# Kernel tuning notes

Measured on AMD Instinct MI355X. Metric: run time of the kernel, lower is better.

## Reference

```python
import jax, jax.numpy as jnp
import numpy as np

SKIP_THRESHOLD = 0.3
NUM_HEADS = 16
TOP_K = 2


def _layernorm(x, g, b, eps=1e-6):
    m = jnp.mean(x, axis=-1, keepdims=True)
    v = jnp.var(x, axis=-1, keepdims=True)
    return (x - m) * jax.lax.rsqrt(v + eps) * g + b


def _silu(x):
    return x * jax.nn.sigmoid(x)


def _causal_dwconv(x, w):
    # x: [B,S,C], w: [k,C] depthwise causal conv
    k, S = w.shape[0], x.shape[1]
    xp = jnp.pad(x, ((0, 0), (k - 1, 0), (0, 0)))
    return sum(xp[:, i:i + S, :] * w[i] for i in range(k))


def _same_dwconv(x, w):
    k, S = w.shape[0], x.shape[1]
    pl = k // 2
    xp = jnp.pad(x, ((0, 0), (pl, k - 1 - pl), (0, 0)))
    return sum(xp[:, i:i + S, :] * w[i] for i in range(k))


def _mamba_block(x, w_in, conv_w, a_log, w_bc, w_dt, dt_bias, d_skip, w_out):
    # Selective-scan SSM (Mamba-style), O(L)
    B, S, D = x.shape
    d_inner = conv_w.shape[1]
    n = w_bc.shape[1] // 2
    xz = x @ w_in                                   # [B,S,2*d_inner]
    xc, z = xz[..., :d_inner], xz[..., d_inner:]
    xc = _silu(_causal_dwconv(xc, conv_w))
    bc = xc @ w_bc                                  # [B,S,2n]
    Bt, Ct = bc[..., :n], bc[..., n:]
    dt = jax.nn.softplus(xc * w_dt + dt_bias)       # [B,S,d_inner]
    A = -jnp.exp(a_log)                             # [d_inner]

    def step(h, inp):
        xc_t, dt_t, B_t, C_t = inp                  # [B,d_inner],[B,d_inner],[B,n],[B,n]
        decay = jnp.exp(dt_t * A)[..., None]        # [B,d_inner,1]
        h = decay * h + (dt_t * xc_t)[..., None] * B_t[:, None, :]
        y_t = jnp.einsum('bcn,bn->bc', h, C_t)
        return h, y_t

    h0 = jnp.zeros((B, d_inner, n), x.dtype)
    xs = (xc.transpose(1, 0, 2), dt.transpose(1, 0, 2),
          Bt.transpose(1, 0, 2), Ct.transpose(1, 0, 2))
    _, ys = jax.lax.scan(step, h0, xs)
    y = ys.transpose(1, 0, 2) + d_skip * xc
    return (y * _silu(z)) @ w_out


def _timecrystal_block(x, theta, w, b):
    # Energy-conserving rotation-style mixing
    return jnp.cos(theta) * x + jnp.sin(theta) * jnp.tanh(x @ w + b)


def _wlam_block(x, wq, wk, wv, wo, conv_w, nh):
    # Haar wavelet decomposition -> attention on approx coeffs -> reconstruct
    B, S, D = x.shape
    hd = D // nh
    inv = 0.7071067811865476
    xe, xo = x[:, 0::2], x[:, 1::2]
    a = (xe + xo) * inv                             # approx [B,S/2,D]
    det = (xe - xo) * inv                           # detail
    L = a.shape[1]
    q = (a @ wq).reshape(B, L, nh, hd)
    k = (a @ wk).reshape(B, L, nh, hd)
    v = (a @ wv).reshape(B, L, nh, hd)
    att = jnp.einsum('bqhd,bkhd->bhqk', q, k) * (1.0 / np.sqrt(hd))
    att = jax.nn.softmax(att, axis=-1)
    o = jnp.einsum('bhqk,bkhd->bqhd', att, v).reshape(B, L, D) @ wo
    xe2 = (o + det) * inv
    xo2 = (o - det) * inv
    y = jnp.stack([xe2, xo2], axis=2).reshape(B, S, D)
    return _same_dwconv(y, conv_w)


def _moe_block(x, wg, w1, b1, w2, b2, top_k):
    # Top-k sparse MoE; dense per-expert compute weighted by top-k gates
    B, S, D = x.shape
    E = wg.shape[1]
    xt = x.reshape(-1, D)
    logits = xt @ wg
    topv, topi = jax.lax.top_k(logits, top_k)
    w = jax.nn.softmax(topv, axis=-1)
    gates = (jax.nn.one_hot(topi, E, dtype=x.dtype) * w[..., None]).sum(axis=1)  # [T,E]
    y = jnp.zeros_like(xt)
    for e in range(E):
        h = jax.nn.gelu(xt @ w1[e] + b1[e])
        y = y + gates[:, e:e + 1] * (h @ w2[e] + b2[e])
    return y.reshape(B, S, D)


def setup_inputs() -> dict:
    key = jax.random.key(0)
    ks = jax.random.split(key, 20)
    B, S, D = 2, 2048, 1024
    DI, N, CK = 2 * D, 64, 4
    E, FF = 8, 4096
    NB = 4

    def rn(k, shape, scale=0.02):
        return jax.random.normal(k, shape, dtype=jnp.float32) * scale

    return {
        'hidden_states': jax.random.normal(ks[0], (B, S, D), jnp.float32),
        'router_w': rn(ks[1], (D, NB)),
        'router_b': jnp.zeros((NB,), jnp.float32),
        'ln_g': jnp.ones((NB, D), jnp.float32),
        'ln_b': jnp.zeros((NB, D), jnp.float32),
        'm_win': rn(ks[2], (D, 2 * DI)),
        'm_conv': rn(ks[3], (CK, DI), 0.1),
        'm_alog': jnp.zeros((DI,), jnp.float32),
        'm_wbc': rn(ks[4], (DI, 2 * N)),
        'm_wdt': rn(ks[5], (DI,)),
        'm_dtb': jnp.full((DI,), -1.0, jnp.float32),
        'm_dskip': jnp.ones((DI,), jnp.float32),
        'm_wout': rn(ks[6], (DI, D)),
        'tc_theta': jnp.array(0.5, jnp.float32),
        'tc_w': rn(ks[7], (D, D)),
        'tc_b': jnp.zeros((D,), jnp.float32),
        'w_q': rn(ks[8], (D, D)),
        'w_k': rn(ks[9], (D, D)),
        'w_v': rn(ks[10], (D, D)),
        'w_o': rn(ks[11], (D, D)),
        'wlam_conv': rn(ks[12], (4, D), 0.25),
        'moe_wg': rn(ks[13], (D, E)),
        'moe_w1': rn(ks[14], (E, D, FF)),
        'moe_b1': jnp.zeros((E, FF), jnp.float32),
        'moe_w2': rn(ks[15], (E, FF, D)),
        'moe_b2': jnp.zeros((E, D), jnp.float32),
    }


def reference(hidden_states, router_w, router_b, ln_g, ln_b,
              m_win, m_conv, m_alog, m_wbc, m_wdt, m_dtb, m_dskip, m_wout,
              tc_theta, tc_w, tc_b,
              w_q, w_k, w_v, w_o, wlam_conv,
              moe_wg, moe_w1, moe_b1, moe_w2, moe_b2):
    h = hidden_states
    # Adaptive block router: mean pool -> sigmoid scores -> hard skip mask (inference)
    pooled = jnp.mean(h, axis=1)                     # [B,D]
    scores = jax.nn.sigmoid(pooled @ router_w + router_b)  # [B,4]
    masks = (scores > SKIP_THRESHOLD).astype(h.dtype)

    h = h + masks[:, 0, None, None] * _mamba_block(
        _layernorm(h, ln_g[0], ln_b[0]), m_win, m_conv, m_alog, m_wbc,
        m_wdt, m_dtb, m_dskip, m_wout)
    h = h + masks[:, 1, None, None] * _timecrystal_block(
        _layernorm(h, ln_g[1], ln_b[1]), tc_theta, tc_w, tc_b)
    h = h + masks[:, 2, None, None] * _wlam_block(
        _layernorm(h, ln_g[2], ln_b[2]), w_q, w_k, w_v, w_o, wlam_conv, NUM_HEADS)
    h = h + masks[:, 3, None, None] * _moe_block(
        _layernorm(h, ln_g[3], ln_b[3]), moe_wg, moe_w1, moe_b1, moe_w2, moe_b2, TOP_K)
    return h
```

## Files before the change

### kernel.cpp

```cpp
#include <hip/hip_runtime.h>
#include <math.h>

#define S_LEN   2048
#define B_SZ    2
#define DM      1024
#define DI      2048
#define NST     64
#define LH      1024
#define NH      16
#define HD      64
#define TT      4096
#define NEXP    8
#define FF      4096
#define CHK     1024
#define MAXTILE 72
#define INVR2   0.7071067811865476f
#define CHUNK   128
#define NCH     16

#define OFF_POOLED 0
#define OFF_COUNTS 2048
#define OFF_CURSOR 2056
#define OFF_MASKS  2064
#define OFF_NTILE  2072
// ... 254 lines not shown
                                                 int ldi, int ldo) {
    __shared__ float t[64][65];
    const int tid = threadIdx.x;
    const int k0 = blockIdx.x << 6, n0 = blockIdx.y << 6;
    const int rr = tid >> 4, cc = (tid & 15) << 2;
#pragma unroll
    for (int i = 0; i < 4; ++i) {
        float4 v = *(const float4*)(in + (size_t)(k0 + rr + i * 16) * ldi + n0 + cc);
        *(float4*)&t[rr + i * 16][cc] = v;
    }
    __syncthreads();
#pragma unroll
    for (int i = 0; i < 4; ++i) {
        int n = rr + i * 16;
        ushort4 h4, m4, l4;
        split3v(t[cc + 0][n], h4.x, m4.x, l4.x);
        split3v(t[cc + 1][n], h4.y, m4.y, l4.y);
        split3v(t[cc + 2][n], h4.z, m4.z, l4.z);
        split3v(t[cc + 3][n], h4.w, m4.w, l4.w);
        size_t of = (size_t)(n0 + n) * ldo + k0 + cc;
        *(ushort4*)(oh + of) = h4;
        *(ushort4*)(om + of) = m4;
        *(ushort4*)(ol + of) = l4;
    }
}

__global__ __launch_bounds__(256) void transb_k(const float* __restrict__ in,
                                                unsigned short* __restrict__ out,
                                                int ldi, int ldo,
                                                long inStride, long outStride) {
    __shared__ float t[64][65];
    const int tid = threadIdx.x;
    in  += (size_t)blockIdx.z * inStride;
    out += (size_t)blockIdx.z * outStride;
    const int k0 = blockIdx.x << 6, n0 = blockIdx.y << 6;
    const int rr = tid >> 4, cc = (tid & 15) << 2;
#pragma unroll
    for (int i = 0; i < 4; ++i) {
        float4 v = *(const float4*)(in + (size_t)(k0 + rr + i * 16) * ldi + n0 + cc);
        *(float4*)&t[rr + i * 16][cc] = v;
    }
    __syncthreads();
#pragma unroll
    for (int i = 0; i < 4; ++i) {
        int n = rr + i * 16;
        ushort4 o;
        o.x = f2b(t[cc + 0][n]); o.y = f2b(t[cc + 1][n]);
        o.z = f2b(t[cc + 2][n]); o.w = f2b(t[cc + 3][n]);
        *(ushort4*)(out + (size_t)(n0 + n) * ldo + k0 + cc) = o;
    }
}

__global__ __launch_bounds__(256) void mmx3_k(const unsigned short* __restrict__ Ah,
                                              const unsigned short* __restrict__ Am,
                                              const unsigned short* __restrict__ Al,
                                              const unsigned short* __restrict__ Bh,
                                              const unsigned short* __restrict__ Bm,
                                              const unsigned short* __restrict__ Bl,
                                              float* __restrict__ C,
                                              int lda, int ldb, int ldc, int K) {
    __shared__ unsigned short S[6][4096];
    const int tid = threadIdx.x;
    const int m0 = (int)blockIdx.x << 7, n0 = (int)blockIdx.y << 7;
    size_t aoff[2], boff[2];
    int dst[2];
#pragma unroll
    for (int c = 0; c < 2; ++c) {
        int idx = tid + (c << 8);
        int r = idx >> 2, sd = idx & 3;
        int ks = (sd ^ (r & 3)) << 3;
        aoff[c] = (size_t)(m0 + r) * lda + ks;
        boff[c] = (size_t)(n0 + r) * ldb + ks;
        dst[c] = idx << 3;
    }
    const int lane = tid & 63;
    const int w = tid >> 6, wr = w >> 1, wc = w & 1;
    const int lrow = lane & 15, lgrp = lane >> 4;
    f4_t acc[4][4];
#pragma unroll
    for (int i = 0; i < 4; ++i)
#pragma unroll
        for (int j = 0; j < 4; ++j) acc[i][j] = (f4_t){0.f, 0.f, 0.f, 0.f};
    int ard[4], brd[4];
#pragma unroll
    for (int t4 = 0; t4 < 4; ++t4) {
        int ra = wr * 64 + t4 * 16 + lrow;
        ard[t4] = ra * 32 + ((lgrp ^ (ra & 3)) << 3);
        int rb = wc * 64 + t4 * 16 + lrow;
        brd[t4] = rb * 32 + ((lgrp ^ (rb & 3)) << 3);
    }
    for (int k0 = 0; k0 < K; k0 += 32) {
        __syncthreads();
#pragma unroll
        for (int c = 0; c < 2; ++c) {
            gld16(Ah + aoff[c] + k0, &S[0][dst[c]]);
            gld16(Am + aoff[c] + k0, &S[1][dst[c]]);
            gld16(Al + aoff[c] + k0, &S[2][dst[c]]);
            gld16(Bh + boff[c] + k0, &S[3][dst[c]]);
            gld16(Bm + boff[c] + k0, &S[4][dst[c]]);
            gld16(Bl + boff[c] + k0, &S[5][dst[c]]);
        }
        __syncthreads();
        bf8_t ah4[4], am4[4], al4[4];
#pragma unroll
        for (int t4 = 0; t4 < 4; ++t4) {
            ah4[t4] = *(const bf8_t*)&S[0][ard[t4]];
            am4[t4] = *(const bf8_t*)&S[1][ard[t4]];
            al4[t4] = *(const bf8_t*)&S[2][ard[t4]];
        }
#pragma unroll
        for (int ni = 0; ni < 4; ++ni) {
            bf8_t bh = *(const bf8_t*)&S[3][brd[ni]];
            bf8_t bm = *(const bf8_t*)&S[4][brd[ni]];
            bf8_t bl = *(const bf8_t*)&S[5][brd[ni]];
#pragma unroll
            for (int mi = 0; mi < 4; ++mi) {
                acc[mi][ni] = __builtin_amdgcn_mfma_f32_16x16x32_bf16(ah4[mi], bh, acc[mi][ni], 0, 0, 0);
                acc[mi][ni] = __builtin_amdgcn_mfma_f32_16x16x32_bf16(am4[mi], bh, acc[mi][ni], 0, 0, 0);
                acc[mi][ni] = __builtin_amdgcn_mfma_f32_16x16x32_bf16(al4[mi], bh, acc[mi][ni], 0, 0, 0);
                acc[mi][ni] = __builtin_amdgcn_mfma_f32_16x16x32_bf16(ah4[mi], bm, acc[mi][ni], 0, 0, 0);
                acc[mi][ni] = __builtin_amdgcn_mfma_f32_16x16x32_bf16(am4[mi], bm, acc[mi][ni], 0, 0, 0);
                acc[mi][ni] = __builtin_amdgcn_mfma_f32_16x16x32_bf16(ah4[mi], bl, acc[mi][ni], 0, 0, 0);
            }
        }
    }
#pragma unroll
    for (int mi = 0; mi < 4; ++mi) {
#pragma unroll
        for (int j = 0; j < 4; ++j) {
            int rr = wr * 64 + mi * 16 + lgrp * 4 + j;
#pragma unroll
            for (int ni = 0; ni < 4; ++ni) {
                int col = n0 + wc * 64 + ni * 16 + lrow;
                C[(size_t)(m0 + rr) * ldc + col] = acc[mi][ni][j];
            }
        }
    }
}

template<int MODE>
__global__ __launch_bounds__(256) void mm_k(const unsigned short* __restrict__ A,
                                            const unsigned short* __restrict__ Bt,
                                            void* __restrict__ Cv,
                                            int lda, int ldb, int ldc, int K,
                                            const float* __restrict__ bias, int fofs,
                                            const int* __restrict__ ntile,
                                            const int* __restrict__ tileE,
                                            const int* __restrict__ tileR,
                                            const int* __restrict__ tileC,
                                            const int* __restrict__ rtok) {
    __shared__ unsigned short As[8192];
    __shared__ unsigned short Bs[8192];
    const int tid = threadIdx.x;
    int m0 = 0;
    const int n0 = (int)blockIdx.y << 7;
    int cnt = 128, e = 0, row0 = 0;
    if constexpr (MODE >= 2) {
        if ((int)blockIdx.x >= ntile[0]) return;
        e = tileE[blockIdx.x]; row0 = tileR[blockIdx.x]; cnt = tileC[blockIdx.x];
    } else {
        m0 = (int)blockIdx.x << 7;
    }
    const unsigned short* Bp = Bt;
    if constexpr (MODE >= 2) Bp += (size_t)e << 20;
    size_t aoff[4], boff[4];
#pragma unroll
    for (int c = 0; c < 4; ++c) {
        int r = (tid >> 3) + 32 * c;
        int ks = ((tid & 7) ^ (r & 7)) << 3;
        int gr;
        if constexpr (MODE == 2)      gr = rtok[row0 + (r < cnt ? r : cnt - 1)];
        else if constexpr (MODE >= 3) gr = row0 + (r < cnt ? r : cnt - 1);
        else                          gr = m0 + r;
        aoff[c] = (size_t)gr * lda + ks;
        boff[c] = (size_t)(n0 + r) * ldb + ks;
    }
    const int lane = tid & 63;
    const int w = tid >> 6, wr = w >> 1, wc = w & 1;
    const int lrow = lane & 15, lgrp = lane >> 4;
    f4_t acc[4][4];
#pragma unroll
    for (int i = 0; i < 4; ++i)
#pragma unroll
        for (int j = 0; j < 4; ++j) acc[i][j] = (f4_t){0.f, 0.f, 0.f, 0.f};
    int ard[4][2], brd[4][2];
#pragma unroll
    for (int t4 = 0; t4 < 4; ++t4)
#pragma unroll
        for (int kk = 0; kk < 2; ++kk) {
            int ra = wr * 64 + t4 * 16 + lrow;
            ard[t4][kk] = ra * 64 + (((lgrp + (kk << 2)) ^ (ra & 7)) << 3);
            int rb = wc * 64 + t4 * 16 + lrow;
            brd[t4][kk] = rb * 64 + (((lgrp + (kk << 2)) ^ (rb & 7)) << 3);
        }
    for (int k0 = 0; k0 < K; k0 += 64) {
        __syncthreads();
#pragma unroll
        for (int c = 0; c < 4; ++c)
            gld16(A + aoff[c] + k0, As + c * 2048 + tid * 8);
#pragma unroll
        for (int c = 0; c < 4; ++c)
            gld16(Bp + boff[c] + k0, Bs + c * 2048 + tid * 8);
        __syncthreads();
        bf8_t af[4][2], bfv[4][2];
#pragma unroll
        for (int t4 = 0; t4 < 4; ++t4) {
            af[t4][0]  = *(const bf8_t*)&As[ard[t4][0]];
            af[t4][1]  = *(const bf8_t*)&As[ard[t4][1]];
            bfv[t4][0] = *(const bf8_t*)&Bs[brd[t4][0]];
            bfv[t4][1] = *(const bf8_t*)&Bs[brd[t4][1]];
        }
#pragma unroll
        for (int mi = 0; mi < 4; ++mi)
#pragma unroll
            for (int ni = 0; ni < 4; ++ni) {
                acc[mi][ni] = __builtin_amdgcn_mfma_f32_16x16x32_bf16(af[mi][0], bfv[ni][0], acc[mi][ni], 0, 0, 0);
                acc[mi][ni] = __builtin_amdgcn_mfma_f32_16x16x32_bf16(af[mi][1], bfv[ni][1], acc[mi][ni], 0, 0, 0);
            }
    }
#pragma unroll
    for (int mi = 0; mi < 4; ++mi) {
#pragma unroll
        for (int j = 0; j < 4; ++j) {
            int lr = wr * 64 + mi * 16 + lgrp * 4 + j;
            if constexpr (MODE >= 2) { if (lr >= cnt) continue; }
#pragma unroll
            for (int ni = 0; ni < 4; ++ni) {
                int col = n0 + wc * 64 + ni * 16 + lrow;
                float vv = acc[mi][ni][j];
                if constexpr (MODE == 0) {
                    ((float*)Cv)[(size_t)(m0 + lr) * ldc + col] = vv;
                } else if constexpr (MODE == 1) {
                    ((unsigned short*)Cv)[(size_t)(m0 + lr) * ldc + col] = f2b(vv);
                } else if constexpr (MODE == 2) {
                    float bz = bias[(size_t)e * FF + fofs + col];
                    ((unsigned short*)Cv)[(size_t)(row0 + lr) * ldc + col] = f2b(gelu_tanh(vv + bz));
                } else if constexpr (MODE == 3) {
                    ((float*)Cv)[(size_t)(row0 + lr) * ldc + col] += vv;
                } else {
                    ((float*)Cv)[(size_t)(row0 + lr) * ldc + col] = vv + bias[(size_t)e * DM + col];
                }
            }
        }
    }
}

__global__ __launch_bounds__(256) void gemmsk_f32(const float* __restrict__ A, int lda,
                                                  const float* __restrict__ B, int ldb,
                                                  float* __restrict__ P, int ldc, int Kslab) {
    __shared__ float As[16][68];
    __shared__ float Bs[16][68];
    const int tid = threadIdx.x;
    const int tx = tid & 15, ty = tid >> 4;
    const int m0 = blockIdx.x * 64, n0 = blockIdx.y * 64;
    const int kbeg = blockIdx.z * Kslab, kend = kbeg + Kslab;
    P += (size_t)blockIdx.z * 4096 * 128;
    const int la_r = tid >> 2, la_k = (tid & 3) << 2;
    const int lb_r = tid >> 4, lb_n = (tid & 15) << 2;
    float acc[4][4] = {};
    for (int k0 = kbeg; k0 < kend; k0 += 16) {
        float4 av = *(const float4*)(A + (size_t)(m0 + la_r) * lda + k0 + la_k);
        float4 bv = *(const float4*)(B + (size_t)(k0 + lb_r) * ldb + n0 + lb_n);
        __syncthreads();
        As[la_k + 0][la_r] = av.x; As[la_k + 1][la_r] = av.y;
        As[la_k + 2][la_r] = av.z; As[la_k + 3][la_r] = av.w;
        *(float4*)&Bs[lb_r][lb_n] = bv;
        __syncthreads();
#pragma unroll
        for (int kk = 0; kk < 16; ++kk) {
            float4 a4 = *(const float4*)&As[kk][ty << 2];
            float4 b4 = *(const float4*)&Bs[kk][tx << 2];
            float aa[4] = {a4.x, a4.y, a4.z, a4.w};
            float bb[4] = {b4.x, b4.y, b4.z, b4.w};
#pragma unroll
            for (int i = 0; i < 4; ++i)
#pragma unroll
                for (int j = 0; j < 4; ++j)
                    acc[i][j] = fmaf(aa[i], bb[j], acc[i][j]);
        }
    }
#pragma unroll
    for (int i = 0; i < 4; ++i) {
        int m = m0 + (ty << 2) + i;
        float4 o;
        o.x = acc[i][0]; o.y = acc[i][1]; o.z = acc[i][2]; o.w = acc[i][3];
        *(float4*)(P + (size_t)m * ldc + n0 + (tx << 2)) = o;
    }
}

__global__ __launch_bounds__(256) void wbc_red_k(const float* __restrict__ part,
                                                 float* __restrict__ bc) {
    size_t i = (size_t)blockIdx.x * 256 + threadIdx.x;
    float s = 0.f;
#pragma unroll
    for (int z = 0; z < 8; ++z) s += part[(size_t)z * 524288 + i];
    bc[i] = s;
}

__global__ __launch_bounds__(256) void mamba_conv_k(const float* __restrict__ xz,
                                                    const float* __restrict__ cw,
                                                    float* __restrict__ xc) {
    size_t i = (size_t)blockIdx.x * 256 + threadIdx.x;
    int c = (int)(i & (DI - 1));
    size_t row = i >> 11;
    int s = (int)(row & (S_LEN - 1));
    float acc = 0.f;
#pragma unroll
    for (int t = 0; t < 4; ++t) {
        int ss = s - 3 + t;
        if (ss >= 0) acc = fmaf(cw[t * DI + c], xz[(row - 3 + t) * 4096 + c], acc);
    }
    float sg = 1.f / (1.f + expf(-acc));
    xc[i] = acc * sg;
}

__global__ __launch_bounds__(256) void scan1_k(const float* __restrict__ xc,
                                               const float* __restrict__ bc,
                                               const float* __restrict__ alog,
                                               const float* __restrict__ wdt,
                                               const float* __restrict__ dtb,
                                               float* __restrict__ hend,
                                               float* __restrict__ pprod) {
    const int b = blockIdx.z, k = blockIdx.y;
    const int c = blockIdx.x * 256 + threadIdx.x;
    __shared__ float Bs[CHUNK][64];
    const int s0 = k * CHUNK;
    const float4* bc4 = (const float4*)(bc + ((size_t)(b * S_LEN + s0)) * 128);
    for (int idx = threadIdx.x; idx < CHUNK * 16; idx += 256) {
        int r = idx >> 4, q = idx & 15;
        *(float4*)&Bs[r][q << 2] = bc4[r * 32 + q];
    }
    __syncthreads();
    const float A = -expf(alog[c]);
    const float wdtc = wdt[c], dtbc = dtb[c];
    float hs[NST];
#pragma unroll
    for (int n = 0; n < NST; ++n) hs[n] = 0.f;
    float dtsum = 0.f;
    const float* xcp = xc + ((size_t)(b * S_LEN + s0)) * DI + c;
    for (int s = 0; s < CHUNK; ++s) {
        float xcv = xcp[(size_t)s * DI];
        float t = fmaf(xcv, wdtc, dtbc);
        float dtv = (t > 20.f) ? t : log1pf(expf(t));
        float decay = expf(dtv * A);
        float coef = dtv * xcv;
        dtsum += dtv;
#pragma unroll
        for (int n4 = 0; n4 < 16; ++n4) {
            float4 bv = *(const float4*)&Bs[s][n4 << 2];
            hs[n4 * 4 + 0] = fmaf(decay, hs[n4 * 4 + 0], coef * bv.x);
            hs[n4 * 4 + 1] = fmaf(decay, hs[n4 * 4 + 1], coef * bv.y);
            hs[n4 * 4 + 2] = fmaf(decay, hs[n4 * 4 + 2], coef * bv.z);
            hs[n4 * 4 + 3] = fmaf(decay, hs[n4 * 4 + 3], coef * bv.w);
        }
    }
    float* hp = hend + (((size_t)(b * NCH + k)) * DI + c) * NST;
#pragma unroll
    for (int n = 0; n < NST; n += 4) {
        float4 v; v.x = hs[n]; v.y = hs[n + 1]; v.z = hs[n + 2]; v.w = hs[n + 3];
        *(float4*)(hp + n) = v;
    }
    pprod[((size_t)(b * NCH + k)) * DI + c] = expf(dtsum * A);
}

__global__ __launch_bounds__(256) void scan2_k(const float* __restrict__ hend,
                                               const float* __restrict__ pprod,
                                               float* __restrict__ hin) {
    size_t g = (size_t)blockIdx.x * 256 + threadIdx.x;
    int n = (int)(g & 63);
    int c = (int)((g >> 6) & (DI - 1));
    int b = (int)(g >> 17);
    float h = 0.f;
    for (int k = 0; k < NCH; ++k) {
        size_t base = (size_t)(b * NCH + k) * DI + c;
        hin[base * NST + n] = h;
        h = fmaf(pprod[base], h, hend[base * NST + n]);
    }
}

__global__ __launch_bounds__(256) void scan3_k(float* __restrict__ xcio,
                                               const float* __restrict__ bc,
                                               const float* __restrict__ xz,
                                               const float* __restrict__ alog,
                                               const float* __restrict__ wdt,
                                               const float* __restrict__ dtb,
                                               const float* __restrict__ dskip,
                                               const float* __restrict__ hin) {
    const int b = blockIdx.z, k = blockIdx.y;
    const int c = blockIdx.x * 256 + threadIdx.x;
    __shared__ float Bs[CHUNK][64];
    __shared__ float Cs[CHUNK][64];
    const int s0 = k * CHUNK;
    const float4* bc4 = (const float4*)(bc + ((size_t)(b * S_LEN + s0)) * 128);
    for (int idx = threadIdx.x; idx < CHUNK * 32; idx += 256) {
        int r = idx >> 5, q = idx & 31;
        float4 v = bc4[r * 32 + q];
        if (q < 16) *(float4*)&Bs[r][q << 2] = v;
        else        *(float4*)&Cs[r][(q - 16) << 2] = v;
    }
    __syncthreads();
    const float A = -expf(alog[c]);
    const float wdtc = wdt[c], dtbc = dtb[c], skipc = dskip[c];
    float hs[NST];
    const float* hp = hin + (((size_t)(b * NCH + k)) * DI + c) * NST;
#pragma unroll
    for (int n = 0; n < NST; n += 4) {
        float4 v = *(const float4*)(hp + n);
        hs[n] = v.x; hs[n + 1] = v.y; hs[n + 2] = v.z; hs[n + 3] = v.w;
    }
    float* xcp = xcio + ((size_t)(b * S_LEN + s0)) * DI + c;
    const float* zp = xz + ((size_t)(b * S_LEN + s0)) * 4096 + DI + c;
    for (int s = 0; s < CHUNK; ++s) {
        float xcv = xcp[(size_t)s * DI];
        float t = fmaf(xcv, wdtc, dtbc);
        float dtv = (t > 20.f) ? t : log1pf(expf(t));
        float decay = expf(dtv * A);
        float coef = dtv * xcv;
        float y = 0.f;
#pragma unroll
        for (int n4 = 0; n4 < 16; ++n4) {
            float4 bv = *(const float4*)&Bs[s][n4 << 2];
            float4 cv = *(const float4*)&Cs[s][n4 << 2];
            float h0 = fmaf(decay, hs[n4 * 4 + 0], coef * bv.x);
            float h1 = fmaf(decay, hs[n4 * 4 + 1], coef * bv.y);
            float h2 = fmaf(decay, hs[n4 * 4 + 2], coef * bv.z);
            float h3 = fmaf(decay, hs[n4 * 4 + 3], coef * bv.w);
            hs[n4 * 4 + 0] = h0; hs[n4 * 4 + 1] = h1;
            hs[n4 * 4 + 2] = h2; hs[n4 * 4 + 3] = h3;
            y = fmaf(h0, cv.x, y); y = fmaf(h1, cv.y, y);
            y = fmaf(h2, cv.z, y); y = fmaf(h3, cv.w, y);
        }
        y = fmaf(skipc, xcv, y);
        float z = zp[(size_t)s * 4096];
        float sz = z / (1.f + expf(-z));
        xcp[(size_t)s * DI] = y * sz;
    }
}

__global__ __launch_bounds__(256) void wsplit_k(const float* __restrict__ ln,
                                                unsigned short* __restrict__ ah,
                                                unsigned short* __restrict__ am,
                                                unsigned short* __restrict__ al,
                                                float* __restrict__ det) {
    size_t f = (size_t)blockIdx.x * 256 + threadIdx.x;
    int d4 = (int)(f & 255);
    size_t l = f >> 8;
    size_t b = l >> 10;
    size_t li = l & 1023;
    const float4* ln4 = (const float4*)ln;
    float4 xe = ln4[(b * S_LEN + 2 * li) * 256 + d4];
    float4 xo = ln4[(b * S_LEN + 2 * li + 1) * 256 + d4];
    float4 av, dv;
    av.x = (xe.x + xo.x) * INVR2; dv.x = (xe.x - xo.x) * INVR2;
    av.y = (xe.y + xo.y) * INVR2; dv.y = (xe.y - xo.y) * INVR2;
    av.z = (xe.z + xo.z) * INVR2; dv.z = (xe.z - xo.z) * INVR2;
    av.w = (xe.w + xo.w) * INVR2; dv.w = (xe.w - xo.w) * INVR2;
    ushort4 h4, m4, l4;
    split3q(av, h4, m4, l4);
    ((ushort4*)ah)[f] = h4;
    ((ushort4*)am)[f] = m4;
    ((ushort4*)al)[f] = l4;
    ((float4*)det)[f] = dv;
}

__global__ __launch_bounds__(256) void wlam_attn_k(const float* __restrict__ q,
                                                   const float* __restrict__ k,
                                                   const float* __restrict__ v,
                                                   float* __restrict__ o0,
                                                   float* __restrict__ o1,
                                                   float* __restrict__ ml) {
    __shared__ float Qt[64][68];
    __shared__ float KPt[64][68];
    __shared__ float Vs[64][68];
    const int tid = threadIdx.x;
    const int b = blockIdx.z >> 1, half = blockIdx.z & 1;
    const int hh = blockIdx.y;
    const int q0 = blockIdx.x << 6;
    const int tx = tid & 15, ty = tid >> 4;
    const int sr = tid & 63, sc4 = (tid >> 6) << 4;
    {
        const float* qp = q + ((size_t)(b * LH + q0 + sr)) * DM + hh * HD + sc4;
        float4 v0 = *(const float4*)qp;
        float4 v1 = *(const float4*)(qp + 4);
        float4 v2 = *(const float4*)(qp + 8);
        float4 v3 = *(const float4*)(qp + 12);
        Qt[sc4 + 0][sr] = v0.x;  Qt[sc4 + 1][sr] = v0.y;  Qt[sc4 + 2][sr] = v0.z;  Qt[sc4 + 3][sr] = v0.w;
        Qt[sc4 + 4][sr] = v1.x;  Qt[sc4 + 5][sr] = v1.y;  Qt[sc4 + 6][sr] = v1.z;  Qt[sc4 + 7][sr] = v1.w;
        Qt[sc4 + 8][sr] = v2.x;  Qt[sc4 + 9][sr] = v2.y;  Qt[sc4 + 10][sr] = v2.z; Qt[sc4 + 11][sr] = v2.w;
        Qt[sc4 + 12][sr] = v3.x; Qt[sc4 + 13][sr] = v3.y; Qt[sc4 + 14][sr] = v3.z; Qt[sc4 + 15][sr] = v3.w;
    }
    float mrow[4] = {-INFINITY, -INFINITY, -INFINITY, -INFINITY};
    float lrow[4] = {0.f, 0.f, 0.f, 0.f};
    float oacc[4][4] = {};
    const int c0beg = half << 9;
    for (int c0 = c0beg; c0 < c0beg + 512; c0 += 64) {
        __syncthreads();
        {
            const float* kp = k + ((size_t)(b * LH + c0 + sr)) * DM + hh * HD + sc4;
            float4 v0 = *(const float4*)kp;
            float4 v1 = *(const float4*)(kp + 4);
            float4 v2 = *(const float4*)(kp + 8);
            float4 v3 = *(const float4*)(kp + 12);
            KPt[sc4 + 0][sr] = v0.x;  KPt[sc4 + 1][sr] = v0.y;  KPt[sc4 + 2][sr] = v0.z;  KPt[sc4 + 3][sr] = v0.w;
            KPt[sc4 + 4][sr] = v1.x;  KPt[sc4 + 5][sr] = v1.y;  KPt[sc4 + 6][sr] = v1.z;  KPt[sc4 + 7][sr] = v1.w;
            KPt[sc4 + 8][sr] = v2.x;  KPt[sc4 + 9][sr] = v2.y;  KPt[sc4 + 10][sr] = v2.z; KPt[sc4 + 11][sr] = v2.w;
            KPt[sc4 + 12][sr] = v3.x; KPt[sc4 + 13][sr] = v3.y; KPt[sc4 + 14][sr] = v3.z; KPt[sc4 + 15][sr] = v3.w;
            const float* vp = v + ((size_t)(b * LH + c0 + sr)) * DM + hh * HD + sc4;
            *(float4*)&Vs[sr][sc4 + 0]  = *(const float4*)vp;
            *(float4*)&Vs[sr][sc4 + 4]  = *(const float4*)(vp + 4);
            *(float4*)&Vs[sr][sc4 + 8]  = *(const float4*)(vp + 8);
            *(float4*)&Vs[sr][sc4 + 12] = *(const float4*)(vp + 12);
        }
        __syncthreads();
        float s[4][4] = {};
#pragma unroll
        for (int d = 0; d < 64; ++d) {
            float4 a4 = *(const float4*)&Qt[d][ty << 2];
            float4 b4 = *(const float4*)&KPt[d][tx << 2];
            float aa[4] = {a4.x, a4.y, a4.z, a4.w};
            float bb[4] = {b4.x, b4.y, b4.z, b4.w};
#pragma unroll
            for (int i = 0; i < 4; ++i)
#pragma unroll
                for (int j = 0; j < 4; ++j)
                    s[i][j] = fmaf(aa[i], bb[j], s[i][j]);
        }
        float rm[4], mn[4], corr[4], rs[4];
#pragma unroll
        for (int i = 0; i < 4; ++i) {
            s[i][0] *= 0.125f; s[i][1] *= 0.125f; s[i][2] *= 0.125f; s[i][3] *= 0.125f;
            rm[i] = fmaxf(fmaxf(s[i][0], s[i][1]), fmaxf(s[i][2], s[i][3]));
        }
#pragma unroll
        for (int off = 8; off; off >>= 1) {
#pragma unroll
            for (int i = 0; i < 4; ++i) rm[i] = fmaxf(rm[i], __shfl_xor(rm[i], off));
        }
#pragma unroll
        for (int i = 0; i < 4; ++i) {
            mn[i] = fmaxf(mrow[i], rm[i]);
            corr[i] = expf(mrow[i] - mn[i]);
            mrow[i] = mn[i];
            s[i][0] = expf(s[i][0] - mn[i]); s[i][1] = expf(s[i][1] - mn[i]);
            s[i][2] = expf(s[i][2] - mn[i]); s[i][3] = expf(s[i][3] - mn[i]);
            rs[i] = (s[i][0] + s[i][1]) + (s[i][2] + s[i][3]);
        }
#pragma unroll
        for (int off = 8; off; off >>= 1) {
#pragma unroll
            for (int i = 0; i < 4; ++i) rs[i] += __shfl_xor(rs[i], off);
        }
#pragma unroll
        for (int i = 0; i < 4; ++i) {
            lrow[i] = lrow[i] * corr[i] + rs[i];
            oacc[i][0] *= corr[i]; oacc[i][1] *= corr[i];
            oacc[i][2] *= corr[i]; oacc[i][3] *= corr[i];
        }
        __syncthreads();
#pragma unroll
        for (int j = 0; j < 4; ++j) {
            float4 pv; pv.x = s[0][j]; pv.y = s[1][j]; pv.z = s[2][j]; pv.w = s[3][j];
            *(float4*)&KPt[(tx << 2) + j][ty << 2] = pv;
        }
        __syncthreads();
#pragma unroll
        for (int kk = 0; kk < 64; ++kk) {
            float4 pa = *(const float4*)&KPt[kk][ty << 2];
            float4 vb = *(const float4*)&Vs[kk][tx << 2];
            float aa[4] = {pa.x, pa.y, pa.z, pa.w};
            float bb[4] = {vb.x, vb.y, vb.z, vb.w};
#pragma unroll
            for (int i = 0; i < 4; ++i)
#pragma unroll
                for (int j = 0; j < 4; ++j)
                    oacc[i][j] = fmaf(aa[i], bb[j], oacc[i][j]);
        }
    }
    float* op = half ? o1 : o0;
#pragma unroll
    for (int i = 0; i < 4; ++i) {
        int rrow = q0 + (ty << 2) + i;
        float4 ov;
        ov.x = oacc[i][0]; ov.y = oacc[i][1]; ov.z = oacc[i][2]; ov.w = oacc[i][3];
        *(float4*)(op + ((size_t)(b * LH + rrow)) * DM + hh * HD + (tx << 2)) = ov;
        if (tx == 0) {
            size_t mi = (size_t)half * 65536 + ((size_t)(b * LH + rrow) * NH + hh) * 2;
            ml[mi] = mrow[i];
            ml[mi + 1] = lrow[i];
        }
    }
}

__global__ __launch_bounds__(256) void attn_merge_k(const float* __restrict__ o0,
                                                    const float* __restrict__ o1,
                                                    const float* __restrict__ ml,
                                                    unsigned short* __restrict__ ph,
                                                    unsigned short* __restrict__ pm,
                                                    unsigned short* __restrict__ pl) {
    int row = blockIdx.x;
    int t = threadIdx.x;
    int hh = t >> 4;
    size_t idx = ((size_t)row * NH + hh) * 2;
    float m0 = ml[idx], l0 = ml[idx + 1];
    float m1 = ml[65536 + idx], l1 = ml[65536 + idx + 1];
    float m = fmaxf(m0, m1);
    float w0 = expf(m0 - m), w1 = expf(m1 - m);
    float inv = 1.f / (l0 * w0 + l1 * w1);
    float4 a = ((const float4*)(o0 + (size_t)row * DM))[t];
    float4 bv = ((const float4*)(o1 + (size_t)row * DM))[t];
    float4 o;
    o.x = (a.x * w0 + bv.x * w1) * inv;
    o.y = (a.y * w0 + bv.y * w1) * inv;
    o.z = (a.z * w0 + bv.z * w1) * inv;
    o.w = (a.w * w0 + bv.w * w1) * inv;
    ushort4 h4, m4, l4;
    split3q(o, h4, m4, l4);
    size_t f = (size_t)row * 256 + t;
    ((ushort4*)ph)[f] = h4;
    ((ushort4*)pm)[f] = m4;
    ((ushort4*)pl)[f] = l4;
}

__global__ __launch_bounds__(256) void moe_gate_k(const float* __restrict__ X,
                                                  const float* __restrict__ wg,
                                                  int* __restrict__ toke,
                                                  float* __restrict__ tokw) {
    const int wv = threadIdx.x >> 6, lane = threadIdx.x & 63;
    const int t = blockIdx.x * 4 + wv;
    const float* x = X + (size_t)t * DM;
    float acc[8] = {0, 0, 0, 0, 0, 0, 0, 0};
    for (int d = lane; d < DM; d += 64) {
        float xv = x[d];
        const float4* wg4 = (const float4*)(wg + (size_t)d * 8);
        float4 wa = wg4[0], wb = wg4[1];
        acc[0] = fmaf(xv, wa.x, acc[0]); acc[1] = fmaf(xv, wa.y, acc[1]);
        acc[2] = fmaf(xv, wa.z, acc[2]); acc[3] = fmaf(xv, wa.w, acc[3]);
        acc[4] = fmaf(xv, wb.x, acc[4]); acc[5] = fmaf(xv, wb.y, acc[5]);
        acc[6] = fmaf(xv, wb.z, acc[6]); acc[7] = fmaf(xv, wb.w, acc[7]);
    }
#pragma unroll
    for (int off = 32; off; off >>= 1) {
#pragma unroll
        for (int j = 0; j < 8; ++j) acc[j] += __shfl_xor(acc[j], off);
    }
    if (lane == 0) {
        int i0 = 0; float v0 = acc[0];
#pragma unroll
        for (int e2 = 1; e2 < 8; ++e2) if (acc[e2] > v0) { v0 = acc[e2]; i0 = e2; }
        int i1 = -1; float v1 = -INFINITY;
#pragma unroll
        for (int e2 = 0; e2 < 8; ++e2) if (e2 != i0 && acc[e2] > v1) { v1 = acc[e2]; i1 = e2; }
        float r = expf(v1 - v0);
        float den = 1.f + r;
        toke[2 * t] = i0; toke[2 * t + 1] = i1;
        tokw[2 * t] = 1.f / den; tokw[2 * t + 1] = r / den;
    }
}

__global__ __launch_bounds__(256) void moe_count_k(const int* __restrict__ toke, int* __restrict__ counts) {
    int t = blockIdx.x * 256 + threadIdx.x;
    atomicAdd(&counts[toke[2 * t]], 1);
    atomicAdd(&counts[toke[2 * t + 1]], 1);
}

__global__ void moe_tiles_k(const int* __restrict__ counts, int* __restrict__ ntile,
                            int* __restrict__ eoff, int* __restrict__ tileE,
                            int* __restrict__ tileR, int* __restrict__ tileC) {
    if (threadIdx.x == 0 && blockIdx.x == 0) {
        int off = 0, nt = 0;
        for (int e = 0; e < NEXP; ++e) {
            eoff[e] = off;
            int c = counts[e];
            for (int r = 0; r < c; r += 128) {
                tileE[nt] = e;
                tileR[nt] = off + r;
                tileC[nt] = (c - r < 128) ? (c - r) : 128;
                ++nt;
            }
            off += c;
        }
        ntile[0] = nt;
    }
}

__global__ __launch_bounds__(256) void moe_place_k(const int* __restrict__ toke,
                                                   const float* __restrict__ tokw,
                                                   const int* __restrict__ eoff,
                                                   int* __restrict__ cursor,
                                                   int* __restrict__ rtok,
                                                   float* __restrict__ rgate,
                                                   int* __restrict__ rexp,
                                                   int* __restrict__ rowof) {
    int t = blockIdx.x * 256 + threadIdx.x;
#pragma unroll
    for (int kk = 0; kk < 2; ++kk) {
        int e = toke[2 * t + kk];
        float wv = tokw[2 * t + kk];
        int r = eoff[e] + atomicAdd(&cursor[e], 1);
        rtok[r] = t; rgate[r] = wv; rexp[r] = e;
        rowof[2 * t + kk] = r;
    }
}

__global__ __launch_bounds__(256) void moe_combine_k(float* __restrict__ h,
                                                     const float* __restrict__ P,
                                                     const int* __restrict__ rowof,
                                                     const float* __restrict__ rgate,
                                                     const float* __restrict__ masks) {
    int t = blockIdx.x;
    int r0 = rowof[2 * t], r1 = rowof[2 * t + 1];
    float g0 = rgate[r0], g1 = rgate[r1];
    float m = masks[(t >> 11) * 4 + 3];
    float4 a = ((const float4*)(P + (size_t)r0 * DM))[threadIdx.x];
    float4 bq = ((const float4*)(P + (size_t)r1 * DM))[threadIdx.x];
    float4* h4 = (float4*)(h + (size_t)t * DM);
    float4 hv = h4[threadIdx.x];
    hv.x += m * (g0 * a.x + g1 * bq.x);
    hv.y += m * (g0 * a.y + g1 * bq.y);
    hv.z += m * (g0 * a.z + g1 * bq.z);
    hv.w += m * (g0 * a.w + g1 * bq.w);
    h4[threadIdx.x] = hv;
}

extern "C" void kernel_launch(void* const* d_in, const int* in_sizes, int n_in,
                              void* d_out, int out_size, void* d_ws, size_t ws_size,
                              hipStream_t stream) {
    const float* hidden    = (const float*)d_in[0];
    const float* router_w  = (const float*)d_in[1];
    const float* router_b  = (const float*)d_in[2];
    const float* ln_g      = (const float*)d_in[3];
    const float* ln_b      = (const float*)d_in[4];
    const float* m_win     = (const float*)d_in[5];
    const float* m_conv    = (const float*)d_in[6];
    const float* m_alog    = (const float*)d_in[7];
    const float* m_wbc     = (const float*)d_in[8];
    const float* m_wdt     = (const float*)d_in[9];
    const float* m_dtb     = (const float*)d_in[10];
    const float* m_dskip   = (const float*)d_in[11];
    const float* m_wout    = (const float*)d_in[12];
    const float* tc_theta  = (const float*)d_in[13];
    const float* tc_w      = (const float*)d_in[14];
    const float* tc_b      = (const float*)d_in[15];
    const float* w_q       = (const float*)d_in[16];
    const float* w_k       = (const float*)d_in[17];
    const float* w_v       = (const float*)d_in[18];
    const float* w_o       = (const float*)d_in[19];
    const float* wlam_cv   = (const float*)d_in[20];
    const float* moe_wg    = (const float*)d_in[21];
    const float* moe_w1    = (const float*)d_in[22];
    const float* moe_b1    = (const float*)d_in[23];
    const float* moe_w2    = (const float*)d_in[24];
    const float* moe_b2    = (const float*)d_in[25];
    float* h = (float*)d_out;
    float* w = (float*)d_ws;
    unsigned short* BIGH = (unsigned short*)(w + OFF_BIG);
    unsigned short* XCU  = (unsigned short*)(w + OFF_XC);
    unsigned short* OUTU = (unsigned short*)(w + OFF_OUT);
#define UPB(F) (BIGH + 2 * (size_t)(F))
#define UPX(F) (XCU  + 2 * (size_t)(F))
#define UPO(F) (OUTU + 2 * (size_t)(F))

    hipMemsetAsync(d_ws, 0, 2064 * sizeof(float), stream);

    pooled_k<<<dim3(4, 2, 16), 256, 0, stream>>>(hidden, w + OFF_POOLED);
    router_k<<<1, 256, 0, stream>>>(w + OFF_POOLED, router_w, router_b, w + OFF_MASKS);

    ln0_copy_k<<<TT, 256, 0, stream>>>(hidden, ln_g + 0 * DM, ln_b + 0 * DM, h,
                                       UPX(0), UPX(2097152), UPX(4194304));
    transb3_k<<<dim3(16, 64), 256, 0, stream>>>(m_win, UPO(0), UPO(2097152), UPX(6291456), 4096, 1024);
    mmx3_k<<<dim3(32, 32), 256, 0, stream>>>(UPX(0), UPX(2097152), UPX(4194304),
                                             UPO(0), UPO(2097152), UPX(6291456),
                                             w + OFF_BIG, 1024, 1024, 4096, 1024);
    mamba_conv_k<<<32768, 256, 0, stream>>>(w + OFF_BIG, m_conv, w + OFF_XC);
    gemmsk_f32<<<dim3(64, 2, 8), 256, 0, stream>>>(w + OFF_XC, DI, m_wbc, 128, w + OFF_LN, 128, 256);
    wbc_red_k<<<2048, 256, 0, stream>>>(w + OFF_LN, w + OFF_BC);
    scan1_k<<<dim3(8, NCH, B_SZ), 256, 0, stream>>>(w + OFF_XC, w + OFF_BC,
                                                    m_alog, m_wdt, m_dtb,
                                                    w + OFF_LN, w + OFF_PPROD);
    scan2_k<<<1024, 256, 0, stream>>>(w + OFF_LN, w + OFF_PPROD, w + OFF_OUT);
    scan3_k<<<dim3(8, NCH, B_SZ), 256, 0, stream>>>(w + OFF_XC, w + OFF_BC, w + OFF_BIG,
                                                    m_alog, m_wdt, m_dtb, m_dskip,
                                                    w + OFF_OUT);
    split3_k<<<8192, 256, 0, stream>>>(w + OFF_XC, UPB(0), UPB(4194304), UPB(8388608));
    transb3_k<<<dim3(32, 16), 256, 0, stream>>>(m_wout, UPB(12582912), UPB(13631488), UPB(14680064), 1024, 2048);
    mmx3_k<<<dim3(32, 8), 256, 0, stream>>>(UPB(0), UPB(4194304), UPB(8388608),
                                            UPB(12582912), UPB(13631488), UPB(14680064),
                                            w + OFF_OUT, 2048, 2048, 1024, 2048);
    add_ln_k<<<TT, 256, 0, stream>>>(h, w + OFF_OUT, w + OFF_MASKS, 0,
                                     ln_g + 1 * DM, ln_b + 1 * DM, w + OFF_LN,
                                     UPB(0), UPB(2097152), UPB(4194304));

    transb3_k<<<dim3(16, 16), 256, 0, stream>>>(tc_w, UPB(6291456), UPB(6815744), UPB(7340032), 1024, 1024);
    mmx3_k<<<dim3(32, 8), 256, 0, stream>>>(UPB(0), UPB(2097152), UPB(4194304),
                                            UPB(6291456), UPB(6815744), UPB(7340032),
                                            w + OFF_OUT, 1024, 1024, 1024, 1024);
    tc_ln_k<<<TT, 256, 0, stream>>>(h, w + OFF_LN, w + OFF_OUT, tc_b, tc_theta, w + OFF_MASKS,
                                    ln_g + 2 * DM, ln_b + 2 * DM, w + OFF_LN);

    float* wdet = w + OFF_BIG;
    wsplit_k<<<2048, 256, 0, stream>>>(w + OFF_LN, UPB(4194304), UPB(5242880), UPB(6291456), wdet);
    transb3_k<<<dim3(16, 16), 256, 0, stream>>>(w_q, UPB(7340032),  UPB(7864320),  UPB(8388608),  1024, 1024);
    transb3_k<<<dim3(16, 16), 256, 0, stream>>>(w_k, UPB(8912896),  UPB(9437184),  UPB(9961472),  1024, 1024);
    transb3_k<<<dim3(16, 16), 256, 0, stream>>>(w_v, UPB(10485760), UPB(11010048), UPB(11534336), 1024, 1024);
    transb3_k<<<dim3(16, 16), 256, 0, stream>>>(w_o, UPB(12058624), UPB(12582912), UPB(13107200), 1024, 1024);
    float* wq_ = w + OFF_XC;
    float* wk_ = w + OFF_XC + 2097152;
    float* wv_ = w + OFF_XC + 4194304;
    float* wo0 = w + OFF_XC + 6291456;
    float* wo1 = w + OFF_OUT;
    float* wml = w + OFF_OUT + 2097152;
    mmx3_k<<<dim3(16, 8), 256, 0, stream>>>(UPB(4194304), UPB(5242880), UPB(6291456),
                                            UPB(7340032), UPB(7864320), UPB(8388608),
                                            wq_, 1024, 1024, 1024, 1024);
    mmx3_k<<<dim3(16, 8), 256, 0, stream>>>(UPB(4194304), UPB(5242880), UPB(6291456),
                                            UPB(8912896), UPB(9437184), UPB(9961472),
                                            wk_, 1024, 1024, 1024, 1024);
    mmx3_k<<<dim3(16, 8), 256, 0, stream>>>(UPB(4194304), UPB(5242880), UPB(6291456),
                                            UPB(10485760), UPB(11010048), UPB(11534336),
                                            wv_, 1024, 1024, 1024, 1024);
    wlam_attn_k<<<dim3(16, NH, B_SZ * 2), 256, 0, stream>>>(wq_, wk_, wv_, wo0, wo1, wml);
    attn_merge_k<<<2048, 256, 0, stream>>>(wo0, wo1, wml,
                                           UPB(13631488), UPB(14680064), UPB(15728640));
    mmx3_k<<<dim3(16, 8), 256, 0, stream>>>(UPB(13631488), UPB(14680064), UPB(15728640),
                                            UPB(12058624), UPB(12582912), UPB(13107200),
                                            w + OFF_OUT, 1024, 1024, 1024, 1024);
    wpost_ln_k<<<TT, 256, 0, stream>>>(h, w + OFF_OUT, wdet, wlam_cv, w + OFF_MASKS,
                                       ln_g + 3 * DM, ln_b + 3 * DM, w + OFF_LN,
                                       UPB(MB_LNB));

    moe_gate_k<<<1024, 256, 0, stream>>>(w + OFF_LN, moe_wg, (int*)(w + OFF_TOKE), w + OFF_TOKW);
    moe_count_k<<<16, 256, 0, stream>>>((const int*)(w + OFF_TOKE), (int*)(w + OFF_COUNTS));
    moe_tiles_k<<<1, 64, 0, stream>>>((const int*)(w + OFF_COUNTS), (int*)(w + OFF_NTILE),
                                      (int*)(w + OFF_EOFF), (int*)(w + OFF_TILEE),
                                      (int*)(w + OFF_TILER), (int*)(w + OFF_TILEC));
    moe_place_k<<<16, 256, 0, stream>>>((const int*)(w + OFF_TOKE), w + OFF_TOKW,
                                        (const int*)(w + OFF_EOFF), (int*)(w + OFF_CURSOR),
                                        (int*)(w + OFF_RTOK), w + OFF_RGATE,
                                        (int*)(w + OFF_REXP), (int*)(w + OFF_ROWOF));
    for (int ci = 0; ci < 4; ++ci) {
        transb_k<<<dim3(16, 16, NEXP), 256, 0, stream>>>(moe_w1 + (size_t)ci * CHK,
                                                         UPB(MB_W1T),
                                                         FF, 1024, (long)DM * FF, 1024L * 1024L);
        transb_k<<<dim3(16, 16, NEXP), 256, 0, stream>>>(moe_w2 + (size_t)ci * CHK * DM,
                                                         UPB(MB_W2T),
                                                         DM, 1024, (long)FF * DM, 1024L * 1024L);
        mm_k<2><<<dim3(MAXTILE, 8), 256, 0, stream>>>(UPB(MB_LNB), UPB(MB_W1T), UPB(MB_HB),
                                                      1024, 1024, 1024, 1024,
                                                      moe_b1, ci * CHK,
                                                      (const int*)(w + OFF_NTILE), (const int*)(w + OFF_TILEE),
                                                      (const int*)(w + OFF_TILER), (const int*)(w + OFF_TILEC),
                                                      (const int*)(w + OFF_RTOK));
        if (ci == 0) {
            mm_k<4><<<dim3(MAXTILE, 8), 256, 0, stream>>>(UPB(MB_HB), UPB(MB_W2T),
                                                          w + OFF_XC, 1024, 1024, 1024, 1024,
                                                          moe_b2, 0,
                                                          (const int*)(w + OFF_NTILE), (const int*)(w + OFF_TILEE),
                                                          (const int*)(w + OFF_TILER), (const int*)(w + OFF_TILEC),
                                                          nullptr);
        } else {
            mm_k<3><<<dim3(MAXTILE, 8), 256, 0, stream>>>(UPB(MB_HB), UPB(MB_W2T),
                                                          w + OFF_XC, 1024, 1024, 1024, 1024,
                                                          nullptr, 0,
                                                          (const int*)(w + OFF_NTILE), (const int*)(w + OFF_TILEE),
                                                          (const int*)(w + OFF_TILER), (const int*)(w + OFF_TILEC),
                                                          nullptr);
        }
    }
    moe_combine_k<<<4096, 256, 0, stream>>>(h, w + OFF_XC, (const int*)(w + OFF_ROWOF),
                                            w + OFF_RGATE, w + OFF_MASKS);
#undef UPB
#undef UPX
#undef UPO
}
```

Measured before the change: 1.726 ms.

## Fuse QKV projections into one GEMM, reuse conv inputs, separate P buffer

The Q, K and V projection GEMMs are merged into a single GEMM with a 3072-wide output by interleaving the transposed weight splits, and the attention kernel reads from the packed QKV layout. The causal depthwise conv now has each thread produce four consecutive timesteps from seven loaded inputs, cutting redundant global loads and using a quarter of the blocks. The attention kernel writes probabilities to a dedicated shared buffer instead of reusing the K tile, which removes one barrier per tile but adds about 17KB of shared memory per block, possibly lowering occupancy.

```diff
diff --git a/kernel.cpp b/kernel.cpp
--- a/kernel.cpp
+++ b/kernel.cpp
@@ -580,16 +580,30 @@
                                                     float* __restrict__ xc) {
     size_t i = (size_t)blockIdx.x * 256 + threadIdx.x;
     int c = (int)(i & (DI - 1));
-    size_t row = i >> 11;
-    int s = (int)(row & (S_LEN - 1));
-    float acc = 0.f;
-#pragma unroll
-    for (int t = 0; t < 4; ++t) {
-        int ss = s - 3 + t;
-        if (ss >= 0) acc = fmaf(cw[t * DI + c], xz[(row - 3 + t) * 4096 + c], acc);
-    }
-    float sg = 1.f / (1.f + expf(-acc));
-    xc[i] = acc * sg;
+    size_t g = i >> 11;
+    int sg = (int)(g & 511);
+    int b = (int)(g >> 9);
+    int s0 = sg << 2;
+    const float* base = xz + ((size_t)b * S_LEN) * 4096 + c;
+    float x[7];
+#pragma unroll
+    for (int t = 0; t < 7; ++t) {
+        int ss = s0 - 3 + t;
+        x[t] = (ss >= 0) ? base[(size_t)ss * 4096] : 0.f;
+    }
+    float w0 = cw[0 * DI + c], w1 = cw[1 * DI + c];
+    float w2 = cw[2 * DI + c], w3 = cw[3 * DI + c];
+    float* out = xc + ((size_t)(b * S_LEN + s0)) * DI + c;
+#pragma unroll
+    for (int j = 0; j < 4; ++j) {
+        float acc = 0.f;
+        acc = fmaf(w0, x[j + 0], acc);
+        acc = fmaf(w1, x[j + 1], acc);
+        acc = fmaf(w2, x[j + 2], acc);
+        acc = fmaf(w3, x[j + 3], acc);
+        float sg2 = 1.f / (1.f + expf(-acc));
+        out[(size_t)j * DI] = acc * sg2;
+    }
 }
 
 __global__ __launch_bounds__(256) void scan1_k(const float* __restrict__ xc,
@@ -741,15 +755,14 @@
     ((float4*)det)[f] = dv;
 }
 
-__global__ __launch_bounds__(256) void wlam_attn_k(const float* __restrict__ q,
-                                                   const float* __restrict__ k,
-                                                   const float* __restrict__ v,
+__global__ __launch_bounds__(256) void wlam_attn_k(const float* __restrict__ qkv,
                                                    float* __restrict__ o0,
                                                    float* __restrict__ o1,
                                                    float* __restrict__ ml) {
     __shared__ float Qt[64][68];
     __shared__ float KPt[64][68];
     __shared__ float Vs[64][68];
+    __shared__ float Ps[64][68];
     const int tid = threadIdx.x;
     const int b = blockIdx.z >> 1, half = blockIdx.z & 1;
     const int hh = blockIdx.y;
@@ -757,7 +770,7 @@
     const int tx = tid & 15, ty = tid >> 4;
     const int sr = tid & 63, sc4 = (tid >> 6) << 4;
     {
-        const float* qp = q + ((size_t)(b * LH + q0 + sr)) * DM + hh * HD + sc4;
+        const float* qp = qkv + ((size_t)(b * LH + q0 + sr)) * 3072 + hh * HD + sc4;
         float4 v0 = *(const float4*)qp;
         float4 v1 = *(const float4*)(qp + 4);
         float4 v2 = *(const float4*)(qp + 8);
@@ -774,7 +787,7 @@
     for (int c0 = c0beg; c0 < c0beg + 512; c0 += 64) {
         __syncthreads();
         {
-            const float* kp = k + ((size_t)(b * LH + c0 + sr)) * DM + hh * HD + sc4;
+            const float* kp = qkv + ((size_t)(b * LH + c0 + sr)) * 3072 + 1024 + hh * HD + sc4;
             float4 v0 = *(const float4*)kp;
             float4 v1 = *(const float4*)(kp + 4);
             float4 v2 = *(const float4*)(kp + 8);
@@ -783,7 +796,7 @@
             KPt[sc4 + 4][sr] = v1.x;  KPt[sc4 + 5][sr] = v1.y;  KPt[sc4 + 6][sr] = v1.z;  KPt[sc4 + 7][sr] = v1.w;
             KPt[sc4 + 8][sr] = v2.x;  KPt[sc4 + 9][sr] = v2.y;  KPt[sc4 + 10][sr] = v2.z; KPt[sc4 + 11][sr] = v2.w;
             KPt[sc4 + 12][sr] = v3.x; KPt[sc4 + 13][sr] = v3.y; KPt[sc4 + 14][sr] = v3.z; KPt[sc4 + 15][sr] = v3.w;
-            const float* vp = v + ((size_t)(b * LH + c0 + sr)) * DM + hh * HD + sc4;
+            const float* vp = qkv + ((size_t)(b * LH + c0 + sr)) * 3072 + 2048 + hh * HD + sc4;
             *(float4*)&Vs[sr][sc4 + 0]  = *(const float4*)vp;
             *(float4*)&Vs[sr][sc4 + 4]  = *(const float4*)(vp + 4);
             *(float4*)&Vs[sr][sc4 + 8]  = *(const float4*)(vp + 8);
@@ -834,16 +847,15 @@
             oacc[i][0] *= corr[i]; oacc[i][1] *= corr[i];
             oacc[i][2] *= corr[i]; oacc[i][3] *= corr[i];
         }
-        __syncthreads();
 #pragma unroll
         for (int j = 0; j < 4; ++j) {
             float4 pv; pv.x = s[0][j]; pv.y = s[1][j]; pv.z = s[2][j]; pv.w = s[3][j];
-            *(float4*)&KPt[(tx << 2) + j][ty << 2] = pv;
+            *(float4*)&Ps[(tx << 2) + j][ty << 2] = pv;
         }
         __syncthreads();
 #pragma unroll
         for (int kk = 0; kk < 64; ++kk) {
-            float4 pa = *(const float4*)&KPt[kk][ty << 2];
+            float4 pa = *(const float4*)&Ps[kk][ty << 2];
             float4 vb = *(const float4*)&Vs[kk][tx << 2];
             float aa[4] = {pa.x, pa.y, pa.z, pa.w};
             float bb[4] = {vb.x, vb.y, vb.z, vb.w};
@@ -1049,7 +1061,7 @@
     mmx3_k<<<dim3(32, 32), 256, 0, stream>>>(UPX(0), UPX(2097152), UPX(4194304),
                                              UPO(0), UPO(2097152), UPX(6291456),
                                              w + OFF_BIG, 1024, 1024, 4096, 1024);
-    mamba_conv_k<<<32768, 256, 0, stream>>>(w + OFF_BIG, m_conv, w + OFF_XC);
+    mamba_conv_k<<<8192, 256, 0, stream>>>(w + OFF_BIG, m_conv, w + OFF_XC);
     gemmsk_f32<<<dim3(64, 2, 8), 256, 0, stream>>>(w + OFF_XC, DI, m_wbc, 128, w + OFF_LN, 128, 256);
     wbc_red_k<<<2048, 256, 0, stream>>>(w + OFF_LN, w + OFF_BC);
     scan1_k<<<dim3(8, NCH, B_SZ), 256, 0, stream>>>(w + OFF_XC, w + OFF_BC,
@@ -1077,26 +1089,18 @@
 
     float* wdet = w + OFF_BIG;
     wsplit_k<<<2048, 256, 0, stream>>>(w + OFF_LN, UPB(4194304), UPB(5242880), UPB(6291456), wdet);
-    transb3_k<<<dim3(16, 16), 256, 0, stream>>>(w_q, UPB(7340032),  UPB(7864320),  UPB(8388608),  1024, 1024);
-    transb3_k<<<dim3(16, 16), 256, 0, stream>>>(w_k, UPB(8912896),  UPB(9437184),  UPB(9961472),  1024, 1024);
-    transb3_k<<<dim3(16, 16), 256, 0, stream>>>(w_v, UPB(10485760), UPB(11010048), UPB(11534336), 1024, 1024);
+    transb3_k<<<dim3(16, 16), 256, 0, stream>>>(w_q, UPB(7340032), UPB(8912896), UPB(10485760), 1024, 1024);
+    transb3_k<<<dim3(16, 16), 256, 0, stream>>>(w_k, UPB(7864320), UPB(9437184), UPB(11010048), 1024, 1024);
+    transb3_k<<<dim3(16, 16), 256, 0, stream>>>(w_v, UPB(8388608), UPB(9961472), UPB(11534336), 1024, 1024);
     transb3_k<<<dim3(16, 16), 256, 0, stream>>>(w_o, UPB(12058624), UPB(12582912), UPB(13107200), 1024, 1024);
-    float* wq_ = w + OFF_XC;
-    float* wk_ = w + OFF_XC + 2097152;
-    float* wv_ = w + OFF_XC + 4194304;
-    float* wo0 = w + OFF_XC + 6291456;
-    float* wo1 = w + OFF_OUT;
-    float* wml = w + OFF_OUT + 2097152;
-    mmx3_k<<<dim3(16, 8), 256, 0, stream>>>(UPB(4194304), UPB(5242880), UPB(6291456),
-                                            UPB(7340032), UPB(7864320), UPB(8388608),
-                                            wq_, 1024, 1024, 1024, 1024);
-    mmx3_k<<<dim3(16, 8), 256, 0, stream>>>(UPB(4194304), UPB(5242880), UPB(6291456),
-                                            UPB(8912896), UPB(9437184), UPB(9961472),
-                                            wk_, 1024, 1024, 1024, 1024);
-    mmx3_k<<<dim3(16, 8), 256, 0, stream>>>(UPB(4194304), UPB(5242880), UPB(6291456),
-                                            UPB(10485760), UPB(11010048), UPB(11534336),
-                                            wv_, 1024, 1024, 1024, 1024);
-    wlam_attn_k<<<dim3(16, NH, B_SZ * 2), 256, 0, stream>>>(wq_, wk_, wv_, wo0, wo1, wml);
+    float* wqkv = w + OFF_XC;
+    float* wo0  = w + OFF_XC + 6291456;
+    float* wo1  = w + OFF_OUT;
+    float* wml  = w + OFF_OUT + 2097152;
+    mmx3_k<<<dim3(16, 24), 256, 0, stream>>>(UPB(4194304), UPB(5242880), UPB(6291456),
+                                             UPB(7340032), UPB(8912896), UPB(10485760),
+                                             wqkv, 1024, 1024, 3072, 1024);
+    wlam_attn_k<<<dim3(16, NH, B_SZ * 2), 256, 0, stream>>>(wqkv, wo0, wo1, wml);
     attn_merge_k<<<2048, 256, 0, stream>>>(wo0, wo1, wml,
                                            UPB(13631488), UPB(14680064), UPB(15728640));
     mmx3_k<<<dim3(16, 8), 256, 0, stream>>>(UPB(13631488), UPB(14680064), UPB(15728640),
```

Result: faster. 1.678 ms (-2.8%).
